# Performance work log

Measured on AMD Instinct MI355X. Metric: run time of the kernel, lower is better.

The kernel has to match this reference:

```python
import jax, jax.numpy as jnp
import numpy as np
from jax import lax

TAU = 2.0
VTH = 1.0
T = 4

def heaviside(x):
    return (x >= 0.0).astype(x.dtype)

def lif_step(v, x):
    # decay_input=False, v_reset=0: v <- v*(1-1/tau) + x ; hard reset to 0
    v = v * (1.0 - 1.0 / TAU) + x
    s = heaviside(v - VTH)
    v = v * (1.0 - s)
    return v, s

def setup_inputs() -> dict:
    key = jax.random.key(0)
    k = jax.random.split(key, 5)
    B, H, W3, W4 = 128, 64, 8, 32
    cc, N, O = 8, 512, 16
    flat = cc * H * W3 * W4  # 131072
    x = jax.random.normal(k[0], (B, 2, H, W3, W4), dtype=jnp.float32)
    w_conv = jax.random.normal(k[1], (cc, 2, 3, 3), dtype=jnp.float32) / np.sqrt(2 * 9)
    w1 = jax.random.normal(k[2], (N, flat), dtype=jnp.float32) / np.sqrt(flat)
    w2 = jax.random.normal(k[3], (N, N), dtype=jnp.float32) / np.sqrt(N)
    w_out = jax.random.normal(k[4], (O, N), dtype=jnp.float32) / np.sqrt(N)
    return {"x": x, "w_conv": w_conv, "w1": w1, "w2": w2, "w_out": w_out}

def reference(x, w_conv, w1, w2, w_out):
    B = x.shape[0]
    # input.reshape(B, C, -1, W4)
    xr = x.reshape(B, x.shape[1], -1, x.shape[4])  # (B, 2, 512, 32)
    conv_input = lax.conv_general_dilated(
        xr, w_conv, window_strides=(1, 1), padding="SAME",
        dimension_numbers=("NCHW", "OIHW", "NCHW"))  # (B, cc, 512, 32)

    # lifconv applied T times to the same conv_input with persistent state
    def conv_step(v, _):
        return lif_step(v, conv_input)
    _, conv_spikes = lax.scan(conv_step, jnp.zeros_like(conv_input), None, length=T)  # (T,B,cc,H',W')

    N = w1.shape[0]
    def fc_step(carry, s_conv):
        v1, v2 = carry
        z1 = s_conv.reshape(B, -1) @ w1.T
        v1, s1 = lif_step(v1, z1)
        z2 = s1 @ w2.T
        v2, s2 = lif_step(v2, z2)
        return (v1, v2), (s1, s2)

    v0 = (jnp.zeros((B, N), x.dtype), jnp.zeros((B, N), x.dtype))
    _, (s1_rec, s2_rec) = lax.scan(fc_step, v0, conv_spikes)  # (T,B,N) each

    out = s2_rec.mean(axis=0) @ w_out.T  # (B, O)
    conv_spk_rec = jnp.moveaxis(conv_spikes, 0, 1)   # (B,T,cc,H',W')
    input_spk_rec = jnp.moveaxis(s1_rec, 0, 1)       # (B,T,N)
    hidden_spk_rec = jnp.moveaxis(s2_rec, 0, 1)      # (B,T,N)
    return (out, conv_spk_rec, input_spk_rec, hidden_spk_rec)
```

## Files before the change

### kernel.cpp

```cpp
#include <hip/hip_runtime.h>
#include <stdint.h>


#define OFF_CONV  2048ll
#define OFF_IN    67110912ll
#define OFF_HID   67373056ll

typedef short bf16x8 __attribute__((ext_vector_type(8)));
typedef float f32x4  __attribute__((ext_vector_type(4)));

__device__ __forceinline__ unsigned short f2bf(float f) {
  unsigned u = __float_as_uint(f);
  u += 0x7FFFu + ((u >> 16) & 1u);
  return (unsigned short)(u >> 16);
}

__device__ __forceinline__ void expand2(unsigned x, unsigned& o0, unsigned& o1) {
  o0 = (x & 1u) * 0x3F80u | (x & 0x100u) * 0x3F8000u;
  unsigned y = x >> 16;
  o1 = (y & 1u) * 0x3F80u | (y & 0x100u) * 0x3F8000u;
}

__global__ __launch_bounds__(256) void conv_lif_kernel(
    const float* __restrict__ x, const float* __restrict__ wc,
    float* __restrict__ out, unsigned char* __restrict__ patt)
{
  __shared__ float wcs[144];
  int tid = threadIdx.x;
  if (tid < 144) wcs[tid] = wc[tid];
  __syncthreads();

  int idx = blockIdx.x * 256 + tid;
  int b   = idx >> 15;
  int k4  = idx & 32767;
  int co  = k4 >> 12;
  int rem = k4 & 4095;
  int h   = rem >> 3;
  int w0  = (rem & 7) * 4;

  const float* xb = x + (long long)b * 32768;
  float c[4] = {0.f, 0.f, 0.f, 0.f};
#pragma unroll
  for (int ci = 0; ci < 2; ++ci) {
    const float* xc = xb + ci * 16384;
    const float* wk = wcs + co * 18 + ci * 9;
    float win[3][6];
#pragma unroll
    for (int r = 0; r < 3; ++r) {
      int hh = h - 1 + r;
      if (hh >= 0 && hh < 512) {
        const float* row = xc + hh * 32;
        float4 m = *(const float4*)(row + w0);
        win[r][1] = m.x; win[r][2] = m.y; win[r][3] = m.z; win[r][4] = m.w;
        win[r][0] = (w0 > 0)  ? row[w0 - 1] : 0.f;
        win[r][5] = (w0 < 28) ? row[w0 + 4] : 0.f;
      } else {
#pragma unroll
        for (int j = 0; j < 6; ++j) win[r][j] = 0.f;
      }
    }
#pragma unroll
    for (int r = 0; r < 3; ++r)
#pragma unroll
      for (int dw = 0; dw < 3; ++dw) {
        float wgt = wk[r * 3 + dw];
#pragma unroll
        for (int j = 0; j < 4; ++j) c[j] += win[r][j + dw] * wgt;
      }
  }

  int k = co * 16384 + h * 32 + w0;
  float* ob = out + OFF_CONV + (long long)b * 524288 + k;
  float v[4] = {0.f, 0.f, 0.f, 0.f};
  unsigned p[4] = {0, 0, 0, 0};
#pragma unroll
  for (int t = 0; t < 4; ++t) {
    float4 sv;
    float sj[4];
#pragma unroll
    for (int j = 0; j < 4; ++j) {
      v[j] = v[j] * 0.5f + c[j];
      int si = (v[j] >= 1.0f) ? 1 : 0;
      sj[j] = (float)si;
      if (si) v[j] = 0.f;
      p[j] |= (unsigned)si << t;
    }
    sv.x = sj[0]; sv.y = sj[1]; sv.z = sj[2]; sv.w = sj[3];
    *(float4*)(ob + t * 131072) = sv;
  }
  unsigned pb = p[0] | (p[1] << 8) | (p[2] << 16) | (p[3] << 24);
  *(unsigned*)(patt + (long long)b * 131072 + k) = pb;
}

__global__ __launch_bounds__(256) void transpose512(
    const float* __restrict__ w2, float* __restrict__ w2t)
{
  __shared__ float tile[32][33];
  int bx = blockIdx.x & 15, by = blockIdx.x >> 4;
  int tx = threadIdx.x & 31, ty = threadIdx.x >> 5;
#pragma unroll
  for (int i = 0; i < 32; i += 8)
    tile[ty + i][tx] = w2[(by * 32 + ty + i) * 512 + bx * 32 + tx];
  __syncthreads();
#pragma unroll
  for (int i = 0; i < 32; i += 8)
    w2t[(bx * 32 + ty + i) * 512 + by * 32 + tx] = tile[tx][ty + i];
}

__global__ __launch_bounds__(512, 2) void gemm_kernel(
    const unsigned char* __restrict__ patt, const float* __restrict__ w1,
    float* __restrict__ partials, int steps)
{
  __shared__ unsigned short As[4][128][40];
  __shared__ unsigned short Bh[128][40];
  __shared__ unsigned short Bl[128][40];

  const int tid   = threadIdx.x;
  const int nt    = blockIdx.x & 3;
  const int chunk = blockIdx.x >> 2;
  const long long k0 = (long long)chunk * steps * 32;

  const int r  = tid >> 2;
  const int ko = (tid & 3) * 8;

  const unsigned char* pA = patt + (long long)r * 131072 + k0 + ko;
  const float* pB = w1 + (long long)(nt * 128 + r) * 131072 + k0 + ko;

  const int lane = tid & 63;
  const int wid  = tid >> 6;
  const int t    = wid >> 1;
  const int nh   = wid & 1;
  const int l15 = lane & 15, quad = lane >> 4;

  f32x4 acc[8][4];
#pragma unroll
  for (int i = 0; i < 8; ++i)
#pragma unroll
    for (int j = 0; j < 4; ++j) acc[i][j] = (f32x4){0.f, 0.f, 0.f, 0.f};

  for (int s = 0; s < steps; ++s) {
    uint2  pa = *(const uint2*)(pA + s * 32);
    float4 f0 = *(const float4*)(pB + s * 32 + 0);
    float4 f1 = *(const float4*)(pB + s * 32 + 4);

    __syncthreads();

#pragma unroll
    for (int tt = 0; tt < 4; ++tt) {
      unsigned x0 = (pa.x >> tt) & 0x01010101u;
      unsigned x1 = (pa.y >> tt) & 0x01010101u;
      unsigned o0, o1, o2, o3;
      expand2(x0, o0, o1);
      expand2(x1, o2, o3);
      *(uint4*)&As[tt][r][ko] = make_uint4(o0, o1, o2, o3);
    }

    float fv[8] = {f0.x, f0.y, f0.z, f0.w, f1.x, f1.y, f1.z, f1.w};
    unsigned hp[4], lp[4];
#pragma unroll
    for (int i = 0; i < 4; ++i) {
      unsigned short h0 = f2bf(fv[2 * i]);
      unsigned short h1 = f2bf(fv[2 * i + 1]);
      float r0 = fv[2 * i]     - __uint_as_float((unsigned)h0 << 16);
      float r1 = fv[2 * i + 1] - __uint_as_float((unsigned)h1 << 16);
      hp[i] = (unsigned)h0 | ((unsigned)f2bf(r1), 0u) * 0u | ((unsigned)h1 << 16);
      lp[i] = (unsigned)f2bf(r0) | ((unsigned)f2bf(r1) << 16);
    }
    *(uint4*)&Bh[r][ko] = make_uint4(hp[0], hp[1], hp[2], hp[3]);
    *(uint4*)&Bl[r][ko] = make_uint4(lp[0], lp[1], lp[2], lp[3]);

    __syncthreads();

    bf16x8 a[8], bh[4], bl[4];
#pragma unroll
    for (int f = 0; f < 8; ++f)
      a[f] = *(const bf16x8*)&As[t][f * 16 + l15][quad * 8];
#pragma unroll
    for (int f = 0; f < 4; ++f) {
      bh[f] = *(const bf16x8*)&Bh[nh * 64 + f * 16 + l15][quad * 8];
      bl[f] = *(const bf16x8*)&Bl[nh * 64 + f * 16 + l15][quad * 8];
    }
#pragma unroll
    for (int fm = 0; fm < 8; ++fm)
#pragma unroll
      for (int fn = 0; fn < 4; ++fn) {
        acc[fm][fn] = __builtin_amdgcn_mfma_f32_16x16x32_bf16(a[fm], bh[fn], acc[fm][fn], 0, 0, 0);
        acc[fm][fn] = __builtin_amdgcn_mfma_f32_16x16x32_bf16(a[fm], bl[fn], acc[fm][fn], 0, 0, 0);
      }
  }

  float* pc = partials + (long long)chunk * 262144;
#pragma unroll
  for (int fm = 0; fm < 8; ++fm)
#pragma unroll
    for (int fn = 0; fn < 4; ++fn) {
      int m = t * 128 + fm * 16 + quad * 4;
      int n = nt * 128 + nh * 64 + fn * 16 + l15;
#pragma unroll
      for (int rg = 0; rg < 4; ++rg)
        pc[(long long)(m + rg) * 512 + n] = acc[fm][fn][rg];
    }
}

__global__ __launch_bounds__(256) void reduce_kernel(
    const float* __restrict__ partials, float* __restrict__ z1, int S)
{
  int idx = blockIdx.x * 256 + threadIdx.x;
  float a = 0.f;
  for (int c = 0; c < S; ++c) a += partials[(long long)c * 262144 + idx];
  z1[idx] = a;
}

__global__ __launch_bounds__(512) void fc_kernel(
    const float* __restrict__ z1, const float* __restrict__ w2t,
    const float* __restrict__ wout, float* __restrict__ out)
{
  int b = blockIdx.x;
  int n = threadIdx.x;
  __shared__ float s1s[512];
  __shared__ float red[512];

  float v1 = 0.f, v2 = 0.f, ssum = 0.f;
#pragma unroll
  for (int t = 0; t < 4; ++t) {
    float z = z1[((t * 128 + b) << 9) + n];
    v1 = v1 * 0.5f + z;
    float s1 = (v1 >= 1.0f) ? 1.f : 0.f;
    out[OFF_IN + ((long long)b * 4 + t) * 512 + n] = s1;
    if (s1 != 0.f) v1 = 0.f;
    s1s[n] = s1;
    __syncthreads();

    float z2 = 0.f;
#pragma unroll 8
    for (int k = 0; k < 512; ++k)
      z2 += s1s[k] * w2t[(k << 9) + n];
    v2 = v2 * 0.5f + z2;
    float s2 = (v2 >= 1.0f) ? 1.f : 0.f;
    out[OFF_HID + ((long long)b * 4 + t) * 512 + n] = s2;
    if (s2 != 0.f) v2 = 0.f;
    ssum += s2;
    __syncthreads();
  }

  s1s[n] = ssum * 0.25f;
  __syncthreads();

  int o = n & 15, part = n >> 4;
  float p = 0.f;
#pragma unroll
  for (int j = 0; j < 16; ++j)
    p += s1s[part * 16 + j] * wout[o * 512 + part * 16 + j];
  red[n] = p;
  __syncthreads();
  if (n < 16) {
    float a = 0.f;
#pragma unroll
    for (int pp = 0; pp < 32; ++pp) a += red[pp * 16 + n];
    out[b * 16 + n] = a;
  }
}

extern "C" void kernel_launch(void* const* d_in, const int* in_sizes, int n_in,
                              void* d_out, int out_size, void* d_ws, size_t ws_size,
                              hipStream_t stream) {
  const float* x     = (const float*)d_in[0];
  const float* wconv = (const float*)d_in[1];
  const float* w1    = (const float*)d_in[2];
  const float* w2    = (const float*)d_in[3];
  const float* wout  = (const float*)d_in[4];
  float* out = (float*)d_out;
  char* ws = (char*)d_ws;

  unsigned char* patt = (unsigned char*)ws;
  float* w2t      = (float*)(ws + 16777216);
  float* z1       = (float*)(ws + 16777216 + 1048576);
  float* partials = (float*)(ws + 16777216 + 2097152);

  int S = 64;
  while (S > 1 && (size_t)(18874368ull + (size_t)S * 1048576ull) > ws_size) S >>= 1;
  int steps = 4096 / S;

  hipLaunchKernelGGL(conv_lif_kernel, dim3(16384), dim3(256), 0, stream,
                     x, wconv, out, patt);
  hipLaunchKernelGGL(transpose512, dim3(256), dim3(256), 0, stream, w2, w2t);
  hipLaunchKernelGGL(gemm_kernel, dim3(4 * S), dim3(512), 0, stream,
                     patt, w1, partials, steps);
  hipLaunchKernelGGL(reduce_kernel, dim3(1024), dim3(256), 0, stream,
                     partials, z1, S);
  hipLaunchKernelGGL(fc_kernel, dim3(128), dim3(512), 0, stream,
                     z1, w2t, wout, out);
}
```

Measured before the change: 682.7 us.

## Load spike A-fragments directly to registers, double-buffer B in LDS, drop transpose

The GEMM kernel no longer stages the expanded spike matrix in shared memory. Each lane loads its packed spike bytes straight into registers and expands them to bf16 fragments, while the split w1 hi/lo tiles use a double-buffered LDS with next-step register prefetch, so each step needs one barrier instead of two. The conv kernel writes spikes with nontemporal stores. The w2 transpose kernel is removed and fc_kernel reads rows of w2 with float4 loads. The trade-offs are uncoalesced per-lane spike loads with more registers, and strided per-thread row reads of w2 in the fc stage.

```diff
diff --git a/kernel.cpp b/kernel.cpp
--- a/kernel.cpp
+++ b/kernel.cpp
@@ -75,45 +75,27 @@
   unsigned p[4] = {0, 0, 0, 0};
 #pragma unroll
   for (int t = 0; t < 4; ++t) {
-    float4 sv;
-    float sj[4];
+    f32x4 sv;
 #pragma unroll
     for (int j = 0; j < 4; ++j) {
       v[j] = v[j] * 0.5f + c[j];
       int si = (v[j] >= 1.0f) ? 1 : 0;
-      sj[j] = (float)si;
+      sv[j] = (float)si;
       if (si) v[j] = 0.f;
       p[j] |= (unsigned)si << t;
     }
-    sv.x = sj[0]; sv.y = sj[1]; sv.z = sj[2]; sv.w = sj[3];
-    *(float4*)(ob + t * 131072) = sv;
+    __builtin_nontemporal_store(sv, (f32x4*)(ob + t * 131072));
   }
   unsigned pb = p[0] | (p[1] << 8) | (p[2] << 16) | (p[3] << 24);
   *(unsigned*)(patt + (long long)b * 131072 + k) = pb;
-}
-
-__global__ __launch_bounds__(256) void transpose512(
-    const float* __restrict__ w2, float* __restrict__ w2t)
-{
-  __shared__ float tile[32][33];
-  int bx = blockIdx.x & 15, by = blockIdx.x >> 4;
-  int tx = threadIdx.x & 31, ty = threadIdx.x >> 5;
-#pragma unroll
-  for (int i = 0; i < 32; i += 8)
-    tile[ty + i][tx] = w2[(by * 32 + ty + i) * 512 + bx * 32 + tx];
-  __syncthreads();
-#pragma unroll
-  for (int i = 0; i < 32; i += 8)
-    w2t[(bx * 32 + ty + i) * 512 + by * 32 + tx] = tile[tx][ty + i];
 }
 
 __global__ __launch_bounds__(512, 2) void gemm_kernel(
     const unsigned char* __restrict__ patt, const float* __restrict__ w1,
     float* __restrict__ partials, int steps)
 {
-  __shared__ unsigned short As[4][128][40];
-  __shared__ unsigned short Bh[128][40];
-  __shared__ unsigned short Bl[128][40];
+  __shared__ unsigned short Bh[2][128][36];
+  __shared__ unsigned short Bl[2][128][36];
 
   const int tid   = threadIdx.x;
   const int nt    = blockIdx.x & 3;
@@ -122,8 +104,6 @@
 
   const int r  = tid >> 2;
   const int ko = (tid & 3) * 8;
-
-  const unsigned char* pA = patt + (long long)r * 131072 + k0 + ko;
   const float* pB = w1 + (long long)(nt * 128 + r) * 131072 + k0 + ko;
 
   const int lane = tid & 63;
@@ -132,61 +112,76 @@
   const int nh   = wid & 1;
   const int l15 = lane & 15, quad = lane >> 4;
 
+  const unsigned char* pA = patt + (long long)l15 * 131072 + k0 + quad * 8;
+
   f32x4 acc[8][4];
 #pragma unroll
   for (int i = 0; i < 8; ++i)
 #pragma unroll
     for (int j = 0; j < 4; ++j) acc[i][j] = (f32x4){0.f, 0.f, 0.f, 0.f};
 
+  float4 fB0 = *(const float4*)(pB);
+  float4 fB1 = *(const float4*)(pB + 4);
+  uint2 pa[8];
+#pragma unroll
+  for (int f = 0; f < 8; ++f)
+    pa[f] = *(const uint2*)(pA + (long long)f * 2097152);
+
   for (int s = 0; s < steps; ++s) {
-    uint2  pa = *(const uint2*)(pA + s * 32);
-    float4 f0 = *(const float4*)(pB + s * 32 + 0);
-    float4 f1 = *(const float4*)(pB + s * 32 + 4);
+    const int buf = s & 1;
+
+    {
+      float fv[8] = {fB0.x, fB0.y, fB0.z, fB0.w, fB1.x, fB1.y, fB1.z, fB1.w};
+      unsigned hp[4], lp[4];
+#pragma unroll
+      for (int i = 0; i < 4; ++i) {
+        unsigned short h0 = f2bf(fv[2 * i]);
+        unsigned short h1 = f2bf(fv[2 * i + 1]);
+        float r0 = fv[2 * i]     - __uint_as_float((unsigned)h0 << 16);
+        float r1 = fv[2 * i + 1] - __uint_as_float((unsigned)h1 << 16);
+        hp[i] = (unsigned)h0 | ((unsigned)h1 << 16);
+        lp[i] = (unsigned)f2bf(r0) | ((unsigned)f2bf(r1) << 16);
+      }
+      *(uint4*)&Bh[buf][r][ko] = make_uint4(hp[0], hp[1], hp[2], hp[3]);
+      *(uint4*)&Bl[buf][r][ko] = make_uint4(lp[0], lp[1], lp[2], lp[3]);
+    }
+
+    const long long sn = (s + 1 < steps) ? (s + 1) : s;
+    float4 nB0 = *(const float4*)(pB + sn * 32);
+    float4 nB1 = *(const float4*)(pB + sn * 32 + 4);
+    uint2 npa[8];
+#pragma unroll
+    for (int f = 0; f < 8; ++f)
+      npa[f] = *(const uint2*)(pA + (long long)f * 2097152 + sn * 32);
 
     __syncthreads();
 
-#pragma unroll
-    for (int tt = 0; tt < 4; ++tt) {
-      unsigned x0 = (pa.x >> tt) & 0x01010101u;
-      unsigned x1 = (pa.y >> tt) & 0x01010101u;
+    bf16x8 bh[4], bl[4];
+#pragma unroll
+    for (int f = 0; f < 4; ++f) {
+      bh[f] = *(const bf16x8*)&Bh[buf][nh * 64 + f * 16 + l15][quad * 8];
+      bl[f] = *(const bf16x8*)&Bl[buf][nh * 64 + f * 16 + l15][quad * 8];
+    }
+
+#pragma unroll
+    for (int fm = 0; fm < 8; ++fm) {
+      unsigned x0 = (pa[fm].x >> t) & 0x01010101u;
+      unsigned x1 = (pa[fm].y >> t) & 0x01010101u;
       unsigned o0, o1, o2, o3;
       expand2(x0, o0, o1);
       expand2(x1, o2, o3);
-      *(uint4*)&As[tt][r][ko] = make_uint4(o0, o1, o2, o3);
-    }
-
-    float fv[8] = {f0.x, f0.y, f0.z, f0.w, f1.x, f1.y, f1.z, f1.w};
-    unsigned hp[4], lp[4];
-#pragma unroll
-    for (int i = 0; i < 4; ++i) {
-      unsigned short h0 = f2bf(fv[2 * i]);
-      unsigned short h1 = f2bf(fv[2 * i + 1]);
-      float r0 = fv[2 * i]     - __uint_as_float((unsigned)h0 << 16);
-      float r1 = fv[2 * i + 1] - __uint_as_float((unsigned)h1 << 16);
-      hp[i] = (unsigned)h0 | ((unsigned)f2bf(r1), 0u) * 0u | ((unsigned)h1 << 16);
-      lp[i] = (unsigned)f2bf(r0) | ((unsigned)f2bf(r1) << 16);
-    }
-    *(uint4*)&Bh[r][ko] = make_uint4(hp[0], hp[1], hp[2], hp[3]);
-    *(uint4*)&Bl[r][ko] = make_uint4(lp[0], lp[1], lp[2], lp[3]);
-
-    __syncthreads();
-
-    bf16x8 a[8], bh[4], bl[4];
-#pragma unroll
-    for (int f = 0; f < 8; ++f)
-      a[f] = *(const bf16x8*)&As[t][f * 16 + l15][quad * 8];
-#pragma unroll
-    for (int f = 0; f < 4; ++f) {
-      bh[f] = *(const bf16x8*)&Bh[nh * 64 + f * 16 + l15][quad * 8];
-      bl[f] = *(const bf16x8*)&Bl[nh * 64 + f * 16 + l15][quad * 8];
-    }
-#pragma unroll
-    for (int fm = 0; fm < 8; ++fm)
+      union { uint4 u; bf16x8 v; } au;
+      au.u = make_uint4(o0, o1, o2, o3);
 #pragma unroll
       for (int fn = 0; fn < 4; ++fn) {
-        acc[fm][fn] = __builtin_amdgcn_mfma_f32_16x16x32_bf16(a[fm], bh[fn], acc[fm][fn], 0, 0, 0);
-        acc[fm][fn] = __builtin_amdgcn_mfma_f32_16x16x32_bf16(a[fm], bl[fn], acc[fm][fn], 0, 0, 0);
-      }
+        acc[fm][fn] = __builtin_amdgcn_mfma_f32_16x16x32_bf16(au.v, bh[fn], acc[fm][fn], 0, 0, 0);
+        acc[fm][fn] = __builtin_amdgcn_mfma_f32_16x16x32_bf16(au.v, bl[fn], acc[fm][fn], 0, 0, 0);
+      }
+    }
+
+    fB0 = nB0; fB1 = nB1;
+#pragma unroll
+    for (int f = 0; f < 8; ++f) pa[f] = npa[f];
   }
 
   float* pc = partials + (long long)chunk * 262144;
@@ -212,7 +207,7 @@
 }
 
 __global__ __launch_bounds__(512) void fc_kernel(
-    const float* __restrict__ z1, const float* __restrict__ w2t,
+    const float* __restrict__ z1, const float* __restrict__ w2,
     const float* __restrict__ wout, float* __restrict__ out)
 {
   int b = blockIdx.x;
@@ -220,6 +215,7 @@
   __shared__ float s1s[512];
   __shared__ float red[512];
 
+  const float* wrow = w2 + (long long)n * 512;
   float v1 = 0.f, v2 = 0.f, ssum = 0.f;
 #pragma unroll
   for (int t = 0; t < 4; ++t) {
@@ -233,8 +229,13 @@
 
     float z2 = 0.f;
 #pragma unroll 8
-    for (int k = 0; k < 512; ++k)
-      z2 += s1s[k] * w2t[(k << 9) + n];
+    for (int k = 0; k < 512; k += 4) {
+      float4 w = *(const float4*)(wrow + k);
+      z2 += s1s[k]     * w.x;
+      z2 += s1s[k + 1] * w.y;
+      z2 += s1s[k + 2] * w.z;
+      z2 += s1s[k + 3] * w.w;
+    }
     v2 = v2 * 0.5f + z2;
     float s2 = (v2 >= 1.0f) ? 1.f : 0.f;
     out[OFF_HID + ((long long)b * 4 + t) * 512 + n] = s2;
@@ -273,21 +274,19 @@
   char* ws = (char*)d_ws;
 
   unsigned char* patt = (unsigned char*)ws;
-  float* w2t      = (float*)(ws + 16777216);
-  float* z1       = (float*)(ws + 16777216 + 1048576);
-  float* partials = (float*)(ws + 16777216 + 2097152);
+  float* z1       = (float*)(ws + 16777216);
+  float* partials = (float*)(ws + 16777216 + 1048576);
 
   int S = 64;
-  while (S > 1 && (size_t)(18874368ull + (size_t)S * 1048576ull) > ws_size) S >>= 1;
+  while (S > 1 && (size_t)(17825792ull + (size_t)S * 1048576ull) > ws_size) S >>= 1;
   int steps = 4096 / S;
 
   hipLaunchKernelGGL(conv_lif_kernel, dim3(16384), dim3(256), 0, stream,
                      x, wconv, out, patt);
-  hipLaunchKernelGGL(transpose512, dim3(256), dim3(256), 0, stream, w2, w2t);
   hipLaunchKernelGGL(gemm_kernel, dim3(4 * S), dim3(512), 0, stream,
                      patt, w1, partials, steps);
   hipLaunchKernelGGL(reduce_kernel, dim3(1024), dim3(256), 0, stream,
                      partials, z1, S);
   hipLaunchKernelGGL(fc_kernel, dim3(128), dim3(512), 0, stream,
-                     z1, w2t, wout, out);
-}
+                     z1, w2, wout, out);
+}
```

Measured after the change: 733.5 us. 1.07x slower.
